# Optimization experiments

Hardware: AMD Instinct MI355X
Metric: run time of the kernel (lower is better)

The kernel has to match this reference:

```python
import jax, jax.numpy as jnp
import numpy as np

N = 50000
E = 800000
D_IN = 128
D_OUT = 128


def setup_inputs() -> dict:
    key = jax.random.key(0)
    ks = jax.random.split(key, 12)
    x = jax.random.normal(ks[0], (N, D_IN), dtype=jnp.float32)
    W1 = jax.random.normal(ks[1], (D_IN, D_OUT), dtype=jnp.float32) * (1.0 / np.sqrt(D_IN))
    b1 = jnp.zeros((D_OUT,), dtype=jnp.float32)
    W2 = jax.random.normal(ks[2], (D_IN, D_OUT), dtype=jnp.float32) * (1.0 / np.sqrt(D_IN))
    b2 = jnp.zeros((D_OUT,), dtype=jnp.float32)
    # inverted-dropout masks, p=0.5 -> values in {0, 2}
    def mask(k):
        return jnp.where(jax.random.uniform(k, (N, D_IN)) < 0.5, 0.0, 2.0).astype(jnp.float32)
    mask_pos1 = mask(ks[3])
    mask_neg1 = mask(ks[4])
    mask_pos2 = mask(ks[5])
    mask_neg2 = mask(ks[6])
    edge_index1 = jax.random.randint(ks[7], (2, E), 0, N, dtype=jnp.int32)
    edge_index2 = jax.random.randint(ks[8], (2, E), 0, N, dtype=jnp.int32)
    perm1 = jax.random.permutation(ks[9], N).astype(jnp.int32)
    perm2 = jax.random.permutation(ks[10], N).astype(jnp.int32)
    return dict(x=x, W1=W1, b1=b1, W2=W2, b2=b2,
                mask_pos1=mask_pos1, mask_neg1=mask_neg1,
                mask_pos2=mask_pos2, mask_neg2=mask_neg2,
                edge_index1=edge_index1, edge_index2=edge_index2,
                perm1=perm1, perm2=perm2)


def gcn_conv(x, W, b, edge_index):
    """PyG GCNConv: add self-loops, symmetric normalization, then x@W aggregation + bias."""
    n = x.shape[0]
    xw = x @ W  # [N, D_OUT]
    loops = jnp.arange(n, dtype=edge_index.dtype)
    src = jnp.concatenate([edge_index[0], loops])
    dst = jnp.concatenate([edge_index[1], loops])
    deg = jax.ops.segment_sum(jnp.ones_like(dst, dtype=xw.dtype), dst, num_segments=n)
    dinv = jax.lax.rsqrt(jnp.maximum(deg, 1.0))  # deg >= 1 due to self-loops
    norm = dinv[src] * dinv[dst]                 # [E+N]
    msg = xw[src] * norm[:, None]                # [E+N, D_OUT]
    out = jax.ops.segment_sum(msg, dst, num_segments=n)
    return out + b


def _branch(x, W, b, edge_index, mask_pos, mask_neg, perm):
    pos_h = jax.nn.relu(gcn_conv(x * mask_pos, W, b, edge_index))
    neg_in = (x * mask_neg)[perm]
    neg_h = jax.nn.relu(gcn_conv(neg_in, W, b, edge_index))
    summary = jnp.mean(pos_h, axis=0, keepdims=True)  # [1, D_OUT]
    return pos_h, neg_h, summary


def reference(x, W1, b1, W2, b2, mask_pos1, mask_neg1, mask_pos2, mask_neg2,
              edge_index1, edge_index2, perm1, perm2):
    p1, n1, s1 = _branch(x, W1, b1, edge_index1, mask_pos1, mask_neg1, perm1)
    p2, n2, s2 = _branch(x, W2, b2, edge_index2, mask_pos2, mask_neg2, perm2)
    return (p1, n1, s1, p2, n2, s2)
```

## Files before the change

kernel.cpp:

```cpp
#include <hip/hip_runtime.h>
#include <hip/hip_fp16.h>

#define NN 50000
#define NE 800000
#define D 128
#define NB 196
#define FILL_BLOCKS 1024
#define GEMM_BLOCKS 3128
#define RNG 6250
#define ESL 6250

typedef _Float16 half8_t __attribute__((ext_vector_type(8)));
typedef _Float16 half4_t __attribute__((ext_vector_type(4)));
typedef float f32x4 __attribute__((ext_vector_type(4)));

__global__ void k_init(int* cnt1, int* cnt2, float* s1, float* s2) {
    int i = blockIdx.x * blockDim.x + threadIdx.x;
    int stride = gridDim.x * blockDim.x;
    for (int j = i; j < NN; j += stride) { cnt1[j] = 0; cnt2[j] = 0; }
    if (i < D) { s1[i] = 0.f; s2[i] = 0.f; }
}

__global__ void k_count(const int* __restrict__ dst1, const int* __restrict__ dst2,
                        int* cnt1, int* cnt2) {
    int r = blockIdx.x & 7;
    int rank = blockIdx.x >> 3;
    unsigned lo = r * RNG;
    int base = rank * ESL;
    for (int e = base + threadIdx.x; e < base + ESL; e += 256) {
        int d1 = dst1[e];
        if ((unsigned)(d1 - lo) < RNG) atomicAdd(&cnt1[d1], 1);
        int d2 = dst2[e];
        if ((unsigned)(d2 - lo) < RNG) atomicAdd(&cnt2[d2], 1);
    }
}

__global__ void k_part(const int* __restrict__ cnt1, const int* __restrict__ cnt2,
                       int* part1, int* part2) {
    __shared__ int sm1[256], sm2[256];
    int t = threadIdx.x;
    int idx = blockIdx.x * 256 + t;
    int v1 = (idx < NN) ? cnt1[idx] : 0;
    int v2 = (idx < NN) ? cnt2[idx] : 0;
    sm1[t] = v1; sm2[t] = v2;
    __syncthreads();
    for (int off = 128; off > 0; off >>= 1) {
        if (t < off) { sm1[t] += sm1[t + off]; sm2[t] += sm2[t + off]; }
        __syncthreads();
    }
    if (t == 0) { part1[blockIdx.x] = sm1[0]; part2[blockIdx.x] = sm2[0]; }
}

__global__ void k_scanp(int* part1, int* part2) {
    __shared__ int sm1[256], sm2[256];
    int t = threadIdx.x;
    int v1 = (t < NB) ? part1[t] : 0;
    int v2 = (t < NB) ? part2[t] : 0;
    sm1[t] = v1; sm2[t] = v2;
    __syncthreads();
    for (int off = 1; off < 256; off <<= 1) {
        int a1 = (t >= off) ? sm1[t - off] : 0;
        int a2 = (t >= off) ? sm2[t - off] : 0;
        __syncthreads();
        sm1[t] += a1; sm2[t] += a2;
        __syncthreads();
    }
    if (t < NB) { part1[t] = sm1[t] - v1; part2[t] = sm2[t] - v2; }
}

__global__ void k_apply(const int* __restrict__ cnt1, const int* __restrict__ cnt2,
                        const int* __restrict__ part1, const int* __restrict__ part2,
                        int* rp1, int* rp2, int* cur1, int* cur2,
                        float* dinv1, float* dinv2) {
    __shared__ int sm1[256], sm2[256];
    int b = blockIdx.x, t = threadIdx.x;
    int idx = b * 256 + t;
    int v1 = (idx < NN) ? cnt1[idx] : 0;
    int v2 = (idx < NN) ? cnt2[idx] : 0;
    sm1[t] = v1; sm2[t] = v2;
    __syncthreads();
    for (int off = 1; off < 256; off <<= 1) {
        int a1 = (t >= off) ? sm1[t - off] : 0;
        int a2 = (t >= off) ? sm2[t - off] : 0;
        __syncthreads();
        sm1[t] += a1; sm2[t] += a2;
        __syncthreads();
    }
    int e1 = sm1[t] - v1 + part1[b];
    int e2 = sm2[t] - v2 + part2[b];
    if (idx < NN) {
        rp1[idx] = e1; cur1[idx] = e1; dinv1[idx] = rsqrtf((float)(v1 + 1));
        rp2[idx] = e2; cur2[idx] = e2; dinv2[idx] = rsqrtf((float)(v2 + 1));
    } else if (idx == NN) {
        rp1[NN] = e1; rp2[NN] = e2;
    }
}

__launch_bounds__(256)
__global__ void k_fill_gemm(const int* __restrict__ src1, const int* __restrict__ dst1,
                            const int* __restrict__ src2, const int* __restrict__ dst2,
                            int* cur1, int* cur2, int* col1, int* col2,
                            const float* __restrict__ x,
                            const float* __restrict__ W1, const float* __restrict__ W2,
                            const float* __restrict__ mp1, const float* __restrict__ mn1,
                            const float* __restrict__ mp2, const float* __restrict__ mn2,
                            const int* __restrict__ perm1, const int* __restrict__ perm2,
                            const float* __restrict__ dinv1, const float* __restrict__ dinv2,
                            _Float16* xwi1, _Float16* xwi2) {
    __shared__ __align__(16) _Float16 WT[128][136];
    int t = threadIdx.x;

    if (blockIdx.x < FILL_BLOCKS) {
        int r = blockIdx.x & 7;
        int rank = blockIdx.x >> 3;
        unsigned lo = r * RNG;
        int base = rank * ESL;
        for (int e = base + t; e < base + ESL; e += 256) {
            int d1 = dst1[e];
            if ((unsigned)(d1 - lo) < RNG) {
                int p = atomicAdd(&cur1[d1], 1);
                col1[p] = src1[e];
            }
            int d2 = dst2[e];
            if ((unsigned)(d2 - lo) < RNG) {
                int p = atomicAdd(&cur2[d2], 1);
                col2[p] = src2[e];
            }
        }
        return;
    }

    int g = blockIdx.x - FILL_BLOCKS;
    int which = g / 782;
    int bx = g - which * 782;
    const float* W = (which < 2) ? W1 : W2;
    const float* mask = (which == 0) ? mp1 : (which == 1) ? mn1 : (which == 2) ? mp2 : mn2;
    const int* perm = (which == 1) ? perm1 : (which == 3) ? perm2 : nullptr;
    const float* dinv = (which < 2) ? dinv1 : dinv2;
    _Float16* out = ((which < 2) ? xwi1 : xwi2) + ((which & 1) ? 128 : 0);

    for (int i = 0; i < 16; i++) {
        int idx = i * 256 + t;
        int k = idx >> 5;
        int j4 = (idx & 31) * 4;
        float4 w = ((const float4*)W)[idx];
        WT[j4 + 0][k] = (_Float16)w.x;
        WT[j4 + 1][k] = (_Float16)w.y;
        WT[j4 + 2][k] = (_Float16)w.z;
        WT[j4 + 3][k] = (_Float16)w.w;
    }
    __syncthreads();

    int wave = t >> 6;
    int lane = t & 63;
    int quad = lane >> 4;
    int m = lane & 15;
    int tile = bx * 4 + wave;
    if (tile * 16 >= NN) return;

    int row = tile * 16 + m;
    int grow = perm ? perm[row] : row;
    const float* xrow = x + (long)grow * D;
    const float* mrow = mask + (long)grow * D;

    half8_t a[4];
    for (int kk = 0; kk < 4; kk++) {
        int k0 = kk * 32 + quad * 8;
        float4 xa = *(const float4*)(xrow + k0);
        float4 xb = *(const float4*)(xrow + k0 + 4);
        float4 ma = *(const float4*)(mrow + k0);
        float4 mb = *(const float4*)(mrow + k0 + 4);
        a[kk][0] = (_Float16)(xa.x * ma.x);
        a[kk][1] = (_Float16)(xa.y * ma.y);
        a[kk][2] = (_Float16)(xa.z * ma.z);
        a[kk][3] = (_Float16)(xa.w * ma.w);
        a[kk][4] = (_Float16)(xb.x * mb.x);
        a[kk][5] = (_Float16)(xb.y * mb.y);
        a[kk][6] = (_Float16)(xb.z * mb.z);
        a[kk][7] = (_Float16)(xb.w * mb.w);
    }

    int rbase = tile * 16 + quad * 4;
    float ds0 = dinv[rbase + 0], ds1 = dinv[rbase + 1];
    float ds2 = dinv[rbase + 2], ds3 = dinv[rbase + 3];

    for (int nt = 0; nt < 8; nt++) {
        f32x4 acc = {0.f, 0.f, 0.f, 0.f};
        for (int kk = 0; kk < 4; kk++) {
            half8_t b = *(const half8_t*)(&WT[nt * 16 + m][kk * 32 + quad * 8]);
            acc = __builtin_amdgcn_mfma_f32_16x16x32_f16(a[kk], b, acc, 0, 0, 0);
        }
        int n = nt * 16 + m;
        out[(long)(rbase + 0) * 256 + n] = (_Float16)(acc[0] * ds0);
        out[(long)(rbase + 1) * 256 + n] = (_Float16)(acc[1] * ds1);
        out[(long)(rbase + 2) * 256 + n] = (_Float16)(acc[2] * ds2);
        out[(long)(rbase + 3) * 256 + n] = (_Float16)(acc[3] * ds3);
    }
}

__launch_bounds__(256)
__global__ void k_agg(const _Float16* __restrict__ xwi1, const _Float16* __restrict__ xwi2,
                      const int* __restrict__ rp1, const int* __restrict__ col1,
                      const float* __restrict__ dinv1,
                      const int* __restrict__ rp2, const int* __restrict__ col2,
                      const float* __restrict__ dinv2,
                      const float* __restrict__ b1, const float* __restrict__ b2,
                      float* out) {
    int g = blockIdx.y;
    const _Float16* xwi = g ? xwi2 : xwi1;
    const int* rp = g ? rp2 : rp1;
    const int* col = g ? col2 : col1;
    const float* dinv = g ? dinv2 : dinv1;
    const float* bias = g ? b2 : b1;
    float* pos_out = out + (g ? 12800128L : 0L);
    float* neg_out = out + (g ? 19200128L : 6400000L);

    int t = threadIdx.x;
    int wave = t >> 6, lane = t & 63;
    int i = blockIdx.x * 4 + wave;
    if (i >= NN) return;
    int j4 = lane * 4;

    half4_t sv = *(const half4_t*)(xwi + (long)i * 256 + j4);
    float a0 = (float)sv[0], a1 = (float)sv[1], a2 = (float)sv[2], a3 = (float)sv[3];
    int e0 = rp[i], e1 = rp[i + 1];
    int e = e0;
    for (; e + 8 <= e1; e += 8) {
        int s0 = col[e + 0], s1 = col[e + 1], s2 = col[e + 2], s3 = col[e + 3];
        int s4 = col[e + 4], s5 = col[e + 5], s6 = col[e + 6], s7 = col[e + 7];
        half4_t v0 = *(const half4_t*)(xwi + (long)s0 * 256 + j4);
        half4_t v1 = *(const half4_t*)(xwi + (long)s1 * 256 + j4);
        half4_t v2 = *(const half4_t*)(xwi + (long)s2 * 256 + j4);
        half4_t v3 = *(const half4_t*)(xwi + (long)s3 * 256 + j4);
        half4_t v4 = *(const half4_t*)(xwi + (long)s4 * 256 + j4);
        half4_t v5 = *(const half4_t*)(xwi + (long)s5 * 256 + j4);
        half4_t v6 = *(const half4_t*)(xwi + (long)s6 * 256 + j4);
        half4_t v7 = *(const half4_t*)(xwi + (long)s7 * 256 + j4);
        a0 += (float)v0[0] + (float)v1[0] + (float)v2[0] + (float)v3[0]
            + (float)v4[0] + (float)v5[0] + (float)v6[0] + (float)v7[0];
        a1 += (float)v0[1] + (float)v1[1] + (float)v2[1] + (float)v3[1]
            + (float)v4[1] + (float)v5[1] + (float)v6[1] + (float)v7[1];
        a2 += (float)v0[2] + (float)v1[2] + (float)v2[2] + (float)v3[2]
            + (float)v4[2] + (float)v5[2] + (float)v6[2] + (float)v7[2];
        a3 += (float)v0[3] + (float)v1[3] + (float)v2[3] + (float)v3[3]
            + (float)v4[3] + (float)v5[3] + (float)v6[3] + (float)v7[3];
    }
    for (; e + 4 <= e1; e += 4) {
        int s0 = col[e + 0], s1 = col[e + 1], s2 = col[e + 2], s3 = col[e + 3];
        half4_t v0 = *(const half4_t*)(xwi + (long)s0 * 256 + j4);
        half4_t v1 = *(const half4_t*)(xwi + (long)s1 * 256 + j4);
        half4_t v2 = *(const half4_t*)(xwi + (long)s2 * 256 + j4);
        half4_t v3 = *(const half4_t*)(xwi + (long)s3 * 256 + j4);
        a0 += (float)v0[0] + (float)v1[0] + (float)v2[0] + (float)v3[0];
        a1 += (float)v0[1] + (float)v1[1] + (float)v2[1] + (float)v3[1];
        a2 += (float)v0[2] + (float)v1[2] + (float)v2[2] + (float)v3[2];
        a3 += (float)v0[3] + (float)v1[3] + (float)v2[3] + (float)v3[3];
    }
    for (; e < e1; e++) {
        int s = col[e];
        half4_t v = *(const half4_t*)(xwi + (long)s * 256 + j4);
        a0 += (float)v[0]; a1 += (float)v[1]; a2 += (float)v[2]; a3 += (float)v[3];
    }
    float di = dinv[i];
    int jj = (lane < 32) ? j4 : (j4 - 128);
    const f32x4* bp = (const f32x4*)(bias + jj);
    f32x4 bv = *bp;
    f32x4 o;
    o[0] = fmaxf(0.f, di * a0 + bv[0]);
    o[1] = fmaxf(0.f, di * a1 + bv[1]);
    o[2] = fmaxf(0.f, di * a2 + bv[2]);
    o[3] = fmaxf(0.f, di * a3 + bv[3]);
    float* dst = ((lane < 32) ? pos_out : neg_out) + (long)i * D + jj;
    __builtin_nontemporal_store(o, (f32x4*)dst);
}

__launch_bounds__(256)
__global__ void k_sum(const float* __restrict__ pos1, const float* __restrict__ pos2,
                      float* s1, float* s2) {
    int g = blockIdx.y;
    const float* pos = g ? pos2 : pos1;
    float* s = g ? s2 : s1;
    int t = threadIdx.x;
    int rg = t >> 5;
    int j = (t & 31) * 4;
    float4 acc = {0.f, 0.f, 0.f, 0.f};
    for (int i = blockIdx.x * 8 + rg; i < NN; i += gridDim.x * 8) {
        float4 v = *(const float4*)(pos + (long)i * D + j);
        acc.x += v.x; acc.y += v.y; acc.z += v.z; acc.w += v.w;
    }
    __shared__ float sm[8][128];
    sm[rg][j + 0] = acc.x;
    sm[rg][j + 1] = acc.y;
    sm[rg][j + 2] = acc.z;
    sm[rg][j + 3] = acc.w;
    __syncthreads();
    if (t < 128) {
        float v = 0.f;
        for (int r = 0; r < 8; r++) v += sm[r][t];
        atomicAdd(&s[t], v * (1.0f / NN));
    }
}

extern "C" void kernel_launch(void* const* d_in, const int* in_sizes, int n_in,
                              void* d_out, int out_size, void* d_ws, size_t ws_size,
                              hipStream_t stream) {
    const float* x   = (const float*)d_in[0];
    const float* W1  = (const float*)d_in[1];
    const float* b1  = (const float*)d_in[2];
    const float* W2  = (const float*)d_in[3];
    const float* b2  = (const float*)d_in[4];
    const float* mp1 = (const float*)d_in[5];
    const float* mn1 = (const float*)d_in[6];
    const float* mp2 = (const float*)d_in[7];
    const float* mn2 = (const float*)d_in[8];
    const int* e1 = (const int*)d_in[9];
    const int* e2 = (const int*)d_in[10];
    const int* perm1 = (const int*)d_in[11];
    const int* perm2 = (const int*)d_in[12];
    const int* src1 = e1;       const int* dst1 = e1 + NE;
    const int* src2 = e2;       const int* dst2 = e2 + NE;
    float* out = (float*)d_out;

    char* w = (char*)d_ws;
    _Float16* xwi1 = (_Float16*)w; w += (size_t)NN * 256 * 2;
    _Float16* xwi2 = (_Float16*)w; w += (size_t)NN * 256 * 2;
    int* cnt1 = (int*)w;  w += (size_t)NN * 4;
    int* cnt2 = (int*)w;  w += (size_t)NN * 4;
    int* cur1 = (int*)w;  w += (size_t)NN * 4;
    int* cur2 = (int*)w;  w += (size_t)NN * 4;
    int* rp1 = (int*)w;   w += (size_t)(NN + 4) * 4;
    int* rp2 = (int*)w;   w += (size_t)(NN + 4) * 4;
    int* col1 = (int*)w;  w += (size_t)NE * 4;
    int* col2 = (int*)w;  w += (size_t)NE * 4;
    float* dinv1 = (float*)w; w += (size_t)NN * 4;
    float* dinv2 = (float*)w; w += (size_t)NN * 4;
    int* part1 = (int*)w; w += (size_t)256 * 4;
    int* part2 = (int*)w; w += (size_t)256 * 4;

    float* s1 = out + 12800000L;
    float* s2 = out + 25600128L;
    const float* pos1 = out;
    const float* pos2 = out + 12800128L;

    k_init<<<dim3(256), 256, 0, stream>>>(cnt1, cnt2, s1, s2);
    k_count<<<dim3(1024), 256, 0, stream>>>(dst1, dst2, cnt1, cnt2);
    k_part<<<dim3(NB), 256, 0, stream>>>(cnt1, cnt2, part1, part2);
    k_scanp<<<dim3(1), 256, 0, stream>>>(part1, part2);
    k_apply<<<dim3(NB), 256, 0, stream>>>(cnt1, cnt2, part1, part2,
                                          rp1, rp2, cur1, cur2, dinv1, dinv2);
    k_fill_gemm<<<dim3(FILL_BLOCKS + GEMM_BLOCKS), 256, 0, stream>>>(
        src1, dst1, src2, dst2, cur1, cur2, col1, col2,
        x, W1, W2, mp1, mn1, mp2, mn2, perm1, perm2, dinv1, dinv2, xwi1, xwi2);
    k_agg<<<dim3(12500, 2), 256, 0, stream>>>(xwi1, xwi2,
                                              rp1, col1, dinv1, rp2, col2, dinv2,
                                              b1, b2, out);
    k_sum<<<dim3(128, 2), 256, 0, stream>>>(pos1, pos2, s1, s2);
}
```

Measured before the change: 533.2 us.

## Add XCC-aware dynamic work stealing for CSR fill and wider half8 aggregation

The CSR fill phase changes from a fixed block-to-range mapping to dynamic slice claiming through per-job atomic tickets. Each block starts on the destination range matching its XCC id, so the atomics on cur arrays stay mostly local to one XCC's L2. Separately, the aggregation kernel now uses 16-byte half8 loads, with the two half-waves processing alternate edges and combining results via a shuffle. The risks are ticket-atomic contention, extra barriers in the fill loop, and idle lanes during the final store.

```diff
diff --git a/kernel.cpp b/kernel.cpp
--- a/kernel.cpp
+++ b/kernel.cpp
@@ -9,15 +9,21 @@
 #define GEMM_BLOCKS 3128
 #define RNG 6250
 #define ESL 6250
+#define NSLICE 128
 
 typedef _Float16 half8_t __attribute__((ext_vector_type(8)));
 typedef _Float16 half4_t __attribute__((ext_vector_type(4)));
 typedef float f32x4 __attribute__((ext_vector_type(4)));
 
-__global__ void k_init(int* cnt1, int* cnt2, float* s1, float* s2) {
+__device__ __forceinline__ int xcc_id() {
+    return __builtin_amdgcn_s_getreg((31 << 11) | 20) & 7;
+}
+
+__global__ void k_init(int* cnt1, int* cnt2, int* tick, float* s1, float* s2) {
     int i = blockIdx.x * blockDim.x + threadIdx.x;
     int stride = gridDim.x * blockDim.x;
     for (int j = i; j < NN; j += stride) { cnt1[j] = 0; cnt2[j] = 0; }
+    if (i < 16) tick[i] = 0;
     if (i < D) { s1[i] = 0.f; s2[i] = 0.f; }
 }
 
@@ -99,7 +105,7 @@
 __launch_bounds__(256)
 __global__ void k_fill_gemm(const int* __restrict__ src1, const int* __restrict__ dst1,
                             const int* __restrict__ src2, const int* __restrict__ dst2,
-                            int* cur1, int* cur2, int* col1, int* col2,
+                            int* cur1, int* cur2, int* col1, int* col2, int* tick,
                             const float* __restrict__ x,
                             const float* __restrict__ W1, const float* __restrict__ W2,
                             const float* __restrict__ mp1, const float* __restrict__ mn1,
@@ -111,20 +117,32 @@
     int t = threadIdx.x;
 
     if (blockIdx.x < FILL_BLOCKS) {
-        int r = blockIdx.x & 7;
-        int rank = blockIdx.x >> 3;
-        unsigned lo = r * RNG;
-        int base = rank * ESL;
-        for (int e = base + t; e < base + ESL; e += 256) {
-            int d1 = dst1[e];
-            if ((unsigned)(d1 - lo) < RNG) {
-                int p = atomicAdd(&cur1[d1], 1);
-                col1[p] = src1[e];
-            }
-            int d2 = dst2[e];
-            if ((unsigned)(d2 - lo) < RNG) {
-                int p = atomicAdd(&cur2[d2], 1);
-                col2[p] = src2[e];
+        __shared__ int sslice;
+        int myx = xcc_id();
+        for (int xx = 0; xx < 8; xx++) {
+            int r = (myx + xx) & 7;
+            unsigned lo = r * RNG;
+            for (int gj = 0; gj < 2; gj++) {
+                int job = gj * 8 + r;
+                const int* srcA = gj ? src2 : src1;
+                const int* dstA = gj ? dst2 : dst1;
+                int* curA = gj ? cur2 : cur1;
+                int* colA = gj ? col2 : col1;
+                while (true) {
+                    if (t == 0) sslice = atomicAdd(&tick[job], 1);
+                    __syncthreads();
+                    int s = sslice;
+                    __syncthreads();
+                    if (s >= NSLICE) break;
+                    int base = s * ESL;
+                    for (int e = base + t; e < base + ESL; e += 256) {
+                        int d = dstA[e];
+                        if ((unsigned)(d - lo) < RNG) {
+                            int p = atomicAdd(&curA[d], 1);
+                            colA[p] = srcA[e];
+                        }
+                    }
+                }
             }
         }
         return;
@@ -219,59 +237,73 @@
     int wave = t >> 6, lane = t & 63;
     int i = blockIdx.x * 4 + wave;
     if (i >= NN) return;
-    int j4 = lane * 4;
-
-    half4_t sv = *(const half4_t*)(xwi + (long)i * 256 + j4);
-    float a0 = (float)sv[0], a1 = (float)sv[1], a2 = (float)sv[2], a3 = (float)sv[3];
+    int sub = lane >> 5;
+    int q = lane & 31;
+    int j8 = q * 8;
+
+    float a0 = 0.f, a1 = 0.f, a2 = 0.f, a3 = 0.f;
+    float a4 = 0.f, a5 = 0.f, a6 = 0.f, a7 = 0.f;
+
+    if (sub == 0) {
+        half8_t v = *(const half8_t*)(xwi + (long)i * 256 + j8);
+        a0 += (float)v[0]; a1 += (float)v[1]; a2 += (float)v[2]; a3 += (float)v[3];
+        a4 += (float)v[4]; a5 += (float)v[5]; a6 += (float)v[6]; a7 += (float)v[7];
+    }
+
     int e0 = rp[i], e1 = rp[i + 1];
     int e = e0;
     for (; e + 8 <= e1; e += 8) {
-        int s0 = col[e + 0], s1 = col[e + 1], s2 = col[e + 2], s3 = col[e + 3];
-        int s4 = col[e + 4], s5 = col[e + 5], s6 = col[e + 6], s7 = col[e + 7];
-        half4_t v0 = *(const half4_t*)(xwi + (long)s0 * 256 + j4);
-        half4_t v1 = *(const half4_t*)(xwi + (long)s1 * 256 + j4);
-        half4_t v2 = *(const half4_t*)(xwi + (long)s2 * 256 + j4);
-        half4_t v3 = *(const half4_t*)(xwi + (long)s3 * 256 + j4);
-        half4_t v4 = *(const half4_t*)(xwi + (long)s4 * 256 + j4);
-        half4_t v5 = *(const half4_t*)(xwi + (long)s5 * 256 + j4);
-        half4_t v6 = *(const half4_t*)(xwi + (long)s6 * 256 + j4);
-        half4_t v7 = *(const half4_t*)(xwi + (long)s7 * 256 + j4);
-        a0 += (float)v0[0] + (float)v1[0] + (float)v2[0] + (float)v3[0]
-            + (float)v4[0] + (float)v5[0] + (float)v6[0] + (float)v7[0];
-        a1 += (float)v0[1] + (float)v1[1] + (float)v2[1] + (float)v3[1]
-            + (float)v4[1] + (float)v5[1] + (float)v6[1] + (float)v7[1];
-        a2 += (float)v0[2] + (float)v1[2] + (float)v2[2] + (float)v3[2]
-            + (float)v4[2] + (float)v5[2] + (float)v6[2] + (float)v7[2];
-        a3 += (float)v0[3] + (float)v1[3] + (float)v2[3] + (float)v3[3]
-            + (float)v4[3] + (float)v5[3] + (float)v6[3] + (float)v7[3];
-    }
-    for (; e + 4 <= e1; e += 4) {
-        int s0 = col[e + 0], s1 = col[e + 1], s2 = col[e + 2], s3 = col[e + 3];
-        half4_t v0 = *(const half4_t*)(xwi + (long)s0 * 256 + j4);
-        half4_t v1 = *(const half4_t*)(xwi + (long)s1 * 256 + j4);
-        half4_t v2 = *(const half4_t*)(xwi + (long)s2 * 256 + j4);
-        half4_t v3 = *(const half4_t*)(xwi + (long)s3 * 256 + j4);
-        a0 += (float)v0[0] + (float)v1[0] + (float)v2[0] + (float)v3[0];
-        a1 += (float)v0[1] + (float)v1[1] + (float)v2[1] + (float)v3[1];
-        a2 += (float)v0[2] + (float)v1[2] + (float)v2[2] + (float)v3[2];
-        a3 += (float)v0[3] + (float)v1[3] + (float)v2[3] + (float)v3[3];
-    }
-    for (; e < e1; e++) {
+        int sA = col[e + 0 + sub], sB = col[e + 2 + sub];
+        int sC = col[e + 4 + sub], sD = col[e + 6 + sub];
+        half8_t vA = *(const half8_t*)(xwi + (long)sA * 256 + j8);
+        half8_t vB = *(const half8_t*)(xwi + (long)sB * 256 + j8);
+        half8_t vC = *(const half8_t*)(xwi + (long)sC * 256 + j8);
+        half8_t vD = *(const half8_t*)(xwi + (long)sD * 256 + j8);
+        a0 += (float)vA[0] + (float)vB[0] + (float)vC[0] + (float)vD[0];
+        a1 += (float)vA[1] + (float)vB[1] + (float)vC[1] + (float)vD[1];
+        a2 += (float)vA[2] + (float)vB[2] + (float)vC[2] + (float)vD[2];
+        a3 += (float)vA[3] + (float)vB[3] + (float)vC[3] + (float)vD[3];
+        a4 += (float)vA[4] + (float)vB[4] + (float)vC[4] + (float)vD[4];
+        a5 += (float)vA[5] + (float)vB[5] + (float)vC[5] + (float)vD[5];
+        a6 += (float)vA[6] + (float)vB[6] + (float)vC[6] + (float)vD[6];
+        a7 += (float)vA[7] + (float)vB[7] + (float)vC[7] + (float)vD[7];
+    }
+    for (; e + 2 <= e1; e += 2) {
+        int s = col[e + sub];
+        half8_t v = *(const half8_t*)(xwi + (long)s * 256 + j8);
+        a0 += (float)v[0]; a1 += (float)v[1]; a2 += (float)v[2]; a3 += (float)v[3];
+        a4 += (float)v[4]; a5 += (float)v[5]; a6 += (float)v[6]; a7 += (float)v[7];
+    }
+    if (e < e1 && sub == 0) {
         int s = col[e];
-        half4_t v = *(const half4_t*)(xwi + (long)s * 256 + j4);
+        half8_t v = *(const half8_t*)(xwi + (long)s * 256 + j8);
         a0 += (float)v[0]; a1 += (float)v[1]; a2 += (float)v[2]; a3 += (float)v[3];
-    }
-    float di = dinv[i];
-    int jj = (lane < 32) ? j4 : (j4 - 128);
-    const f32x4* bp = (const f32x4*)(bias + jj);
-    f32x4 bv = *bp;
-    f32x4 o;
-    o[0] = fmaxf(0.f, di * a0 + bv[0]);
-    o[1] = fmaxf(0.f, di * a1 + bv[1]);
-    o[2] = fmaxf(0.f, di * a2 + bv[2]);
-    o[3] = fmaxf(0.f, di * a3 + bv[3]);
-    float* dst = ((lane < 32) ? pos_out : neg_out) + (long)i * D + jj;
-    __builtin_nontemporal_store(o, (f32x4*)dst);
+        a4 += (float)v[4]; a5 += (float)v[5]; a6 += (float)v[6]; a7 += (float)v[7];
+    }
+
+    a0 += __shfl_down(a0, 32); a1 += __shfl_down(a1, 32);
+    a2 += __shfl_down(a2, 32); a3 += __shfl_down(a3, 32);
+    a4 += __shfl_down(a4, 32); a5 += __shfl_down(a5, 32);
+    a6 += __shfl_down(a6, 32); a7 += __shfl_down(a7, 32);
+
+    if (sub == 0) {
+        float di = dinv[i];
+        int jj = (q < 16) ? j8 : (j8 - 128);
+        f32x4 bv0 = *(const f32x4*)(bias + jj);
+        f32x4 bv1 = *(const f32x4*)(bias + jj + 4);
+        f32x4 o0, o1;
+        o0[0] = fmaxf(0.f, di * a0 + bv0[0]);
+        o0[1] = fmaxf(0.f, di * a1 + bv0[1]);
+        o0[2] = fmaxf(0.f, di * a2 + bv0[2]);
+        o0[3] = fmaxf(0.f, di * a3 + bv0[3]);
+        o1[0] = fmaxf(0.f, di * a4 + bv1[0]);
+        o1[1] = fmaxf(0.f, di * a5 + bv1[1]);
+        o1[2] = fmaxf(0.f, di * a6 + bv1[2]);
+        o1[3] = fmaxf(0.f, di * a7 + bv1[3]);
+        float* dst = ((q < 16) ? pos_out : neg_out) + (long)i * D + jj;
+        __builtin_nontemporal_store(o0, (f32x4*)dst);
+        __builtin_nontemporal_store(o1, (f32x4*)(dst + 4));
+    }
 }
 
 __launch_bounds__(256)
@@ -336,20 +368,21 @@
     float* dinv2 = (float*)w; w += (size_t)NN * 4;
     int* part1 = (int*)w; w += (size_t)256 * 4;
     int* part2 = (int*)w; w += (size_t)256 * 4;
+    int* tick  = (int*)w; w += (size_t)16 * 4;
 
     float* s1 = out + 12800000L;
     float* s2 = out + 25600128L;
     const float* pos1 = out;
     const float* pos2 = out + 12800128L;
 
-    k_init<<<dim3(256), 256, 0, stream>>>(cnt1, cnt2, s1, s2);
+    k_init<<<dim3(256), 256, 0, stream>>>(cnt1, cnt2, tick, s1, s2);
     k_count<<<dim3(1024), 256, 0, stream>>>(dst1, dst2, cnt1, cnt2);
     k_part<<<dim3(NB), 256, 0, stream>>>(cnt1, cnt2, part1, part2);
     k_scanp<<<dim3(1), 256, 0, stream>>>(part1, part2);
     k_apply<<<dim3(NB), 256, 0, stream>>>(cnt1, cnt2, part1, part2,
                                           rp1, rp2, cur1, cur2, dinv1, dinv2);
     k_fill_gemm<<<dim3(FILL_BLOCKS + GEMM_BLOCKS), 256, 0, stream>>>(
-        src1, dst1, src2, dst2, cur1, cur2, col1, col2,
+        src1, dst1, src2, dst2, cur1, cur2, col1, col2, tick,
         x, W1, W2, mp1, mn1, mp2, mn2, perm1, perm2, dinv1, dinv2, xwi1, xwi2);
     k_agg<<<dim3(12500, 2), 256, 0, stream>>>(xwi1, xwi2,
                                               rp1, col1, dinv1, rp2, col2, dinv2,
```

Result: slower. 622.0 us (+16.6%).
